# Performance work log

Measured on AMD Instinct MI355X. Metric: run time of the kernel, lower is better.

The kernel has to match this reference:

```python
import jax, jax.numpy as jnp
import numpy as np

DIM = 1024
NUM_HEADS = 16
HEAD_DIM = DIM // NUM_HEADS
SCALE = HEAD_DIM ** -0.5


def setup_inputs() -> dict:
    key = jax.random.key(0)
    k_x, k_qkv, k_pw, k_pb = jax.random.split(key, 4)
    B, L = 2, 2048
    x = jax.random.normal(k_x, (B, L, DIM), dtype=jnp.float32)
    # nn.Linear weights are [out, in]; stored the same way here.
    w_qkv = jax.random.normal(k_qkv, (3 * DIM, DIM), dtype=jnp.float32) * (DIM ** -0.5)
    w_proj = jax.random.normal(k_pw, (DIM, DIM), dtype=jnp.float32) * (DIM ** -0.5)
    b_proj = jax.random.normal(k_pb, (DIM,), dtype=jnp.float32) * 0.01
    return {"x": x, "w_qkv": w_qkv, "w_proj": w_proj, "b_proj": b_proj}


def reference(x, w_qkv, w_proj, b_proj):
    B, L, P = x.shape
    H, D = NUM_HEADS, HEAD_DIM
    # qkv projection (no bias): [B, L, 3*P]
    qkv = jnp.einsum('blp,op->blo', x, w_qkv)
    qkv = qkv.reshape(B, L, 3, H, D).transpose(2, 0, 3, 1, 4)  # [3, B, H, L, D]
    q, k, v = qkv[0], qkv[1], qkv[2]
    attn = jnp.einsum('bhld,bhmd->bhlm', q, k) * SCALE  # [B, H, L, L]
    attn = jax.nn.softmax(attn, axis=-1)
    out = jnp.einsum('bhlm,bhmd->bhld', attn, v)  # [B, H, L, D]
    out = out.transpose(0, 2, 1, 3).reshape(B, L, P)
    out = jnp.einsum('blp,op->blo', out, w_proj) + b_proj
    return out
```

## Files before the change

### kernel.cpp

```cpp
#include <hip/hip_runtime.h>
#include <hip/hip_bf16.h>
#include <stdint.h>
#include <stddef.h>

typedef short s16x8 __attribute__((ext_vector_type(8)));
typedef float f32x4  __attribute__((ext_vector_type(4)));
typedef float f32x16 __attribute__((ext_vector_type(16)));
typedef unsigned int u32x2 __attribute__((ext_vector_type(2)));

#define MFMA16(a, b, c) __builtin_amdgcn_mfma_f32_16x16x32_bf16((a), (b), (c), 0, 0, 0)
#define MFMA32(a, b, c) __builtin_amdgcn_mfma_f32_32x32x16_bf16((a), (b), (c), 0, 0, 0)
#define EXP2(x) __builtin_amdgcn_exp2f(x)
#define FMAX3(a, b, c) fmaxf(fmaxf((a), (b)), (c))

__device__ __forceinline__ unsigned short f2bf(float f) {
  union { float f; uint32_t u; } v; v.f = f;
  uint32_t u = v.u;
  return (unsigned short)((u + 0x7FFFu + ((u >> 16) & 1u)) >> 16);
}

__device__ __forceinline__ unsigned int pack_bf16x2(float a, float b) {
  __hip_bfloat162 h = __float22bfloat162_rn(make_float2(a, b));
  union { __hip_bfloat162 h; unsigned int u; } c; c.h = h;
  return c.u;
}

__device__ __forceinline__ void load_lds16(const void* gsrc, void* ldst) {
  void* gp = const_cast<void*>(gsrc);
  __builtin_amdgcn_global_load_lds(
      (__attribute__((address_space(1))) void*)gp,
      (__attribute__((address_space(3))) void*)ldst, 16, 0, 0);
}

#define B_    2
#define L_    2048
#define DIM_  1024
#define NH_   16
#define HD_   64
#define MTOT  (B_ * L_)
#define QSCALE_ 0.18033688011112042f

__global__ void cvt_all(const float* __restrict__ x, const float* __restrict__ wq,
                        const float* __restrict__ wp,
                        unsigned short* __restrict__ xb, unsigned short* __restrict__ wqb,
                        unsigned short* __restrict__ wpb) {
  const int X4 = 1048576, Q4 = 786432;
  int i = blockIdx.x * 256 + threadIdx.x;
  const float* in; unsigned short* out; int idx;
  if (i < X4)            { in = x;  out = xb;  idx = i; }
  else if (i < X4 + Q4)  { in = wq; out = wqb; idx = i - X4; }
  else                   { in = wp; out = wpb; idx = i - X4 - Q4; }
  float4 v = ((const float4*)in)[idx];
  uint2 r;
  r.x = pack_bf16x2(v.x, v.y);
  r.y = pack_bf16x2(v.z, v.w);
  ((uint2*)out)[idx] = r;
}

template <int EPI>
__global__ void __launch_bounds__(256)
gemm_bt(const unsigned short* __restrict__ A,
        const unsigned short* __restrict__ Bw,
        int M, int N, int K,
        unsigned short* __restrict__ Qb,
        unsigned short* __restrict__ Kb,
        unsigned short* __restrict__ Vt,
        float* __restrict__ Cout,
        const float* __restrict__ bias) {
  __shared__ __attribute__((aligned(16))) unsigned short Al[2][128 * 32];
  __shared__ __attribute__((aligned(16))) unsigned short Bl[2][128 * 32];
  const int tid  = threadIdx.x;
  const int lane = tid & 63, wv = tid >> 6;
  const int g = lane >> 4, lr = lane & 15;
  const int wr = wv >> 1, wc = wv & 1;
  const int m0 = blockIdx.x * 128, n0 = blockIdx.y * 128;

  f32x4 acc[4][4];
  const f32x4 zero = {0.f, 0.f, 0.f, 0.f};
#pragma unroll
  for (int i = 0; i < 4; i++)
#pragma unroll
    for (int j = 0; j < 4; j++) acc[i][j] = zero;

#define STAGE_G(buf, k0)                                                              \
  {                                                                                   \
    _Pragma("unroll")                                                                 \
    for (int pass = 0; pass < 2; ++pass) {                                            \
      int c   = pass * 256 + wv * 64 + lane;                                          \
      int row = c >> 2, kc = c & 3;                                                   \
      int ks  = (kc ^ ((row ^ (row >> 2)) & 3)) * 8;                                  \
      load_lds16(A  + (size_t)(m0 + row) * K + (k0) + ks, (char*)&Al[buf][0] + c * 16); \
      load_lds16(Bw + (size_t)(n0 + row) * K + (k0) + ks, (char*)&Bl[buf][0] + c * 16); \
    }                                                                                 \
  }

  STAGE_G(0, 0);
  __syncthreads();
  const int NTk = K >> 5;
  for (int t = 0; t < NTk; ++t) {
    const int cur = t & 1;
    if (t + 1 < NTk) STAGE_G(cur ^ 1, (t + 1) * 32);

    s16x8 af[4], bf[4];
#pragma unroll
    for (int mi = 0; mi < 4; mi++) {
      int row = wr * 64 + mi * 16 + lr;
      int ch  = g ^ ((row ^ (row >> 2)) & 3);
      af[mi]  = *(const s16x8*)((const char*)&Al[cur][0] + row * 64 + ch * 16);
    }
#pragma unroll
    for (int ni = 0; ni < 4; ni++) {
      int row = wc * 64 + ni * 16 + lr;
      int ch  = g ^ ((row ^ (row >> 2)) & 3);
      bf[ni]  = *(const s16x8*)((const char*)&Bl[cur][0] + row * 64 + ch * 16);
    }
#pragma unroll
    for (int mi = 0; mi < 4; mi++)
#pragma unroll
      for (int ni = 0; ni < 4; ni++)
        acc[mi][ni] = MFMA16(af[mi], bf[ni], acc[mi][ni]);
    __syncthreads();
  }
#undef STAGE_G

  if (EPI == 0) {
#pragma unroll
    for (int mi = 0; mi < 4; mi++)
#pragma unroll
      for (int ni = 0; ni < 4; ni++) {
        int ncol = n0 + wc * 64 + ni * 16 + lr;
        int s = ncol >> 10;
        int h = (ncol >> 6) & 15;
        int d = ncol & 63;
#pragma unroll
        for (int j = 0; j < 4; j++) {
          int m = m0 + wr * 64 + mi * 16 + g * 4 + j;
          int b = m >> 11, l = m & 2047;
          size_t bh = (size_t)(b * NH_ + h);
          if (s == 0)      Qb[(bh * L_ + l) * HD_ + d] = f2bf(acc[mi][ni][j] * QSCALE_);
          else if (s == 1) Kb[(bh * L_ + l) * HD_ + d] = f2bf(acc[mi][ni][j]);
          else             Vt[(bh * HD_ + d) * L_ + l] = f2bf(acc[mi][ni][j]);
        }
      }
  } else {
#pragma unroll
    for (int mi = 0; mi < 4; mi++)
#pragma unroll
      for (int ni = 0; ni < 4; ni++) {
        int ncol = n0 + wc * 64 + ni * 16 + lr;
        float bv = bias[ncol];
#pragma unroll
        for (int j = 0; j < 4; j++) {
          int m = m0 + wr * 64 + mi * 16 + g * 4 + j;
          Cout[(size_t)m * N + ncol] = acc[mi][ni][j] + bv;
        }
      }
  }
}

__global__ void __launch_bounds__(256)
attn_fwd(const unsigned short* __restrict__ Qb,
         const unsigned short* __restrict__ Kb,
         const unsigned short* __restrict__ Vt,
         unsigned short* __restrict__ Ob) {
  __shared__ __attribute__((aligned(16))) unsigned short Kl[2][64 * 64];
  __shared__ __attribute__((aligned(16))) unsigned short Vl[2][64 * 64];

  const int tid  = threadIdx.x;
  const int lane = tid & 63, wv = tid >> 6;
  const int hi = lane >> 5, lq = lane & 31;
  const int qt = blockIdx.x, bh = blockIdx.y;

  const unsigned short* Qh = Qb + (size_t)bh * L_ * HD_;
  const unsigned short* Kh = Kb + (size_t)bh * L_ * HD_;
  const unsigned short* Vh = Vt + (size_t)bh * HD_ * L_;
  const int q0 = qt * 128 + wv * 32;

  s16x8 qf[4];
#pragma unroll
  for (int ks = 0; ks < 4; ++ks)
    qf[ks] = *(const s16x8*)(Qh + (size_t)(q0 + lq) * HD_ + ks * 16 + hi * 8);

  s16x8 onesf;
#pragma unroll
  for (int e = 0; e < 8; ++e) onesf[e] = (short)0x3F80;

  f32x16 o0, o1, o2;
#pragma unroll
  for (int r = 0; r < 16; ++r) { o0[r] = 0.f; o1[r] = 0.f; o2[r] = 0.f; }
  float rm = -1e30f;

#define STAGE(buf, kv0)                                                          \
  {                                                                              \
    _Pragma("unroll")                                                            \
    for (int it = 0; it < 2; ++it) {                                             \
      int c = it * 256 + wv * 64 + lane;                                         \
      int row = c >> 3, cc = c & 7;                                              \
      int cs = (cc ^ (row & 7)) * 8;                                             \
      load_lds16(Kh + (size_t)((kv0) + row) * HD_ + cs, (char*)&Kl[buf][0] + c * 16); \
      load_lds16(Vh + (size_t)row * L_ + (kv0) + cs,    (char*)&Vl[buf][0] + c * 16); \
    }                                                                            \
  }

  STAGE(0, 0);
  __syncthreads();

  const int NT = L_ / 64;
  for (int t = 0; t < NT; ++t) {
    const int cur = t & 1;
    if (t + 1 < NT) STAGE(cur ^ 1, (t + 1) * 64);

    const unsigned short* KL = &Kl[cur][0];
    const unsigned short* VL = &Vl[cur][0];

    f32x16 s0, s1;
#pragma unroll
    for (int r = 0; r < 16; ++r) { s0[r] = 0.f; s1[r] = 0.f; }
    __builtin_amdgcn_s_setprio(1);
#pragma unroll
    for (int ks = 0; ks < 4; ++ks) {
      int cc = ((ks << 1) | hi) ^ (lq & 7);
      s16x8 k0 = *(const s16x8*)((const char*)KL + lq * 128 + cc * 16);
      s0 = MFMA32(k0, qf[ks], s0);
      s16x8 k1 = *(const s16x8*)((const char*)KL + (32 + lq) * 128 + cc * 16);
      s1 = MFMA32(k1, qf[ks], s1);
    }
    __builtin_amdgcn_s_setprio(0);

    float t0, t1, t2, t3, t4, t5;
    {
      float m01 = FMAX3(fmaxf(s0[0], s1[0]), fmaxf(s0[1], s1[1]), fmaxf(s0[2], s1[2]));
      float m02 = FMAX3(fmaxf(s0[3], s1[3]), fmaxf(s0[4], s1[4]), fmaxf(s0[5], s1[5]));
      float m03 = FMAX3(fmaxf(s0[6], s1[6]), fmaxf(s0[7], s1[7]), fmaxf(s0[8], s1[8]));
      float m04 = FMAX3(fmaxf(s0[9], s1[9]), fmaxf(s0[10], s1[10]), fmaxf(s0[11], s1[11]));
      float m05 = FMAX3(fmaxf(s0[12], s1[12]), fmaxf(s0[13], s1[13]), fmaxf(s0[14], s1[14]));
      float m06 = fmaxf(s0[15], s1[15]);
      t0 = FMAX3(m01, m02, m03);
      t1 = FMAX3(m04, m05, m06);
    }
    float pmh = fmaxf(t0, t1);
    union { float f; unsigned u; } cu; cu.f = pmh;
    u32x2 sw = __builtin_amdgcn_permlane32_swap(cu.u, cu.u, false, false);
    union { unsigned u; float f; } ca, cb; ca.u = sw[0]; cb.u = sw[1];
    float pm = fmaxf(ca.f, cb.f);

    float mn = rm;
    if (!__all(pm <= rm + 8.0f)) {
      mn = fmaxf(rm, pm);
      float al = EXP2(rm - mn);
#pragma unroll
      for (int r = 0; r < 16; ++r) { o0[r] *= al; o1[r] *= al; }
      o2[0] *= al;
      rm = mn;
    }

#pragma unroll
    for (int r = 0; r < 16; ++r) { s0[r] = EXP2(s0[r] - mn); s1[r] = EXP2(s1[r] - mn); }

#pragma unroll
    for (int st = 0; st < 2; ++st) {
      unsigned int pd[8];
#pragma unroll
      for (int r2 = 0; r2 < 8; ++r2)
        pd[r2] = st ? pack_bf16x2(s1[2 * r2], s1[2 * r2 + 1])
                    : pack_bf16x2(s0[2 * r2], s0[2 * r2 + 1]);
      __builtin_amdgcn_s_setprio(1);
#pragma unroll
      for (int ksl = 0; ksl < 2; ++ksl) {
        u32x2 e0 = __builtin_amdgcn_permlane32_swap(pd[4 * ksl + 0], pd[4 * ksl + 2], false, false);
        u32x2 e1 = __builtin_amdgcn_permlane32_swap(pd[4 * ksl + 1], pd[4 * ksl + 3], false, false);
        union { unsigned int u[4]; s16x8 v; } pa;
        pa.u[0] = e0[0];
        pa.u[1] = e1[0];
        pa.u[2] = e0[1];
        pa.u[3] = e1[1];
#pragma unroll
        for (int dt = 0; dt < 2; ++dt) {
          int row = dt * 32 + lq;
          int cc = (4 * st + 2 * ksl + hi) ^ (row & 7);
          s16x8 vf = *(const s16x8*)((const char*)VL + row * 128 + cc * 16);
          if (dt == 0) o0 = MFMA32(vf, pa.v, o0);
          else         o1 = MFMA32(vf, pa.v, o1);
        }
        o2 = MFMA32(onesf, pa.v, o2);
      }
      __builtin_amdgcn_s_setprio(0);
    }

    __syncthreads();
  }
#undef STAGE

  const int b = bh >> 4, h = bh & 15;
  const int q = q0 + lq;
  const float inv = 1.0f / o2[0];
  size_t base = ((size_t)(b * L_ + q)) * DIM_ + h * HD_;
#pragma unroll
  for (int dt = 0; dt < 2; ++dt)
#pragma unroll
    for (int r2 = 0; r2 < 8; ++r2) {
      int d = dt * 32 + 8 * (r2 >> 1) + 4 * hi + 2 * (r2 & 1);
      float a = (dt ? o1[2 * r2] : o0[2 * r2]) * inv;
      float c = (dt ? o1[2 * r2 + 1] : o0[2 * r2 + 1]) * inv;
      unsigned int pv = pack_bf16x2(a, c);
      *(unsigned int*)((unsigned short*)Ob + base + d) = pv;
    }
}

extern "C" void kernel_launch(void* const* d_in, const int* in_sizes, int n_in,
                              void* d_out, int out_size, void* d_ws, size_t ws_size,
                              hipStream_t stream) {
  const float* x      = (const float*)d_in[0];
  const float* w_qkv  = (const float*)d_in[1];
  const float* w_proj = (const float*)d_in[2];
  const float* b_proj = (const float*)d_in[3];
  float* out = (float*)d_out;

  const size_t N_X    = (size_t)MTOT * DIM_;
  const size_t N_WQKV = (size_t)3 * DIM_ * DIM_;
  const size_t N_WPRJ = (size_t)DIM_ * DIM_;
  const size_t N_QKV  = (size_t)B_ * NH_ * L_ * HD_;

  unsigned short* xb     = (unsigned short*)d_ws;
  unsigned short* wqkvb  = xb + N_X;
  unsigned short* wprojb = wqkvb + N_WQKV;
  unsigned short* Qb     = wprojb + N_WPRJ;
  unsigned short* Kb     = Qb + N_QKV;
  unsigned short* Vt     = Kb + N_QKV;
  unsigned short* Obuf   = Vt + N_QKV;

  cvt_all<<<8192, 256, 0, stream>>>(x, w_qkv, w_proj, xb, wqkvb, wprojb);

  dim3 g1(MTOT / 128, (3 * DIM_) / 128);
  gemm_bt<0><<<g1, 256, 0, stream>>>(xb, wqkvb, MTOT, 3 * DIM_, DIM_,
                                     Qb, Kb, Vt, nullptr, nullptr);

  dim3 g2(L_ / 128, B_ * NH_);
  attn_fwd<<<g2, 256, 0, stream>>>(Qb, Kb, Vt, Obuf);

  dim3 g3(MTOT / 128, DIM_ / 128);
  gemm_bt<1><<<g3, 256, 0, stream>>>(Obuf, wprojb, MTOT, DIM_, DIM_,
                                     nullptr, nullptr, nullptr, out, b_proj);
}
```

Baseline: 136.4 us.

## Triple-buffer LDS staging with explicit vmcnt waits and one barrier per iteration

Both the GEMM and attention kernels move from double to triple-buffered LDS tiles. Loads are issued two tiles ahead, and each iteration waits only for the older tile with s_waitcnt vmcnt, using a single raw barrier instead of two __syncthreads. This aims to hide global-to-LDS latency better and halve the barrier count. The cost is 50% more LDS per block, which may reduce occupancy, and the vmcnt(4) counting depends on the exact number of loads per stage. The GEMM MFMA block also gets raised wave priority.

```diff
diff --git a/kernel.cpp b/kernel.cpp
--- a/kernel.cpp
+++ b/kernel.cpp
@@ -12,6 +12,14 @@
 #define MFMA32(a, b, c) __builtin_amdgcn_mfma_f32_32x32x16_bf16((a), (b), (c), 0, 0, 0)
 #define EXP2(x) __builtin_amdgcn_exp2f(x)
 #define FMAX3(a, b, c) fmaxf(fmaxf((a), (b)), (c))
+
+#define WAITCNT_VM(N) asm volatile("s_waitcnt vmcnt(" #N ")" ::: "memory")
+#define BARRIER_RAW()                                  \
+  do {                                                 \
+    asm volatile("" ::: "memory");                     \
+    __builtin_amdgcn_s_barrier();                      \
+    asm volatile("" ::: "memory");                     \
+  } while (0)
 
 __device__ __forceinline__ unsigned short f2bf(float f) {
   union { float f; uint32_t u; } v; v.f = f;
@@ -67,8 +75,8 @@
         unsigned short* __restrict__ Vt,
         float* __restrict__ Cout,
         const float* __restrict__ bias) {
-  __shared__ __attribute__((aligned(16))) unsigned short Al[2][128 * 32];
-  __shared__ __attribute__((aligned(16))) unsigned short Bl[2][128 * 32];
+  __shared__ __attribute__((aligned(16))) unsigned short Al[3][128 * 32];
+  __shared__ __attribute__((aligned(16))) unsigned short Bl[3][128 * 32];
   const int tid  = threadIdx.x;
   const int lane = tid & 63, wv = tid >> 6;
   const int g = lane >> 4, lr = lane & 15;
@@ -95,11 +103,14 @@
   }
 
   STAGE_G(0, 0);
-  __syncthreads();
+  STAGE_G(1, 32);
   const int NTk = K >> 5;
   for (int t = 0; t < NTk; ++t) {
-    const int cur = t & 1;
-    if (t + 1 < NTk) STAGE_G(cur ^ 1, (t + 1) * 32);
+    if (t + 1 < NTk) WAITCNT_VM(4);
+    else             WAITCNT_VM(0);
+    BARRIER_RAW();
+    if (t + 2 < NTk) STAGE_G((t + 2) % 3, (t + 2) * 32);
+    const int cur = t % 3;
 
     s16x8 af[4], bf[4];
 #pragma unroll
@@ -114,12 +125,13 @@
       int ch  = g ^ ((row ^ (row >> 2)) & 3);
       bf[ni]  = *(const s16x8*)((const char*)&Bl[cur][0] + row * 64 + ch * 16);
     }
+    __builtin_amdgcn_s_setprio(1);
 #pragma unroll
     for (int mi = 0; mi < 4; mi++)
 #pragma unroll
       for (int ni = 0; ni < 4; ni++)
         acc[mi][ni] = MFMA16(af[mi], bf[ni], acc[mi][ni]);
-    __syncthreads();
+    __builtin_amdgcn_s_setprio(0);
   }
 #undef STAGE_G
 
@@ -163,8 +175,8 @@
          const unsigned short* __restrict__ Kb,
          const unsigned short* __restrict__ Vt,
          unsigned short* __restrict__ Ob) {
-  __shared__ __attribute__((aligned(16))) unsigned short Kl[2][64 * 64];
-  __shared__ __attribute__((aligned(16))) unsigned short Vl[2][64 * 64];
+  __shared__ __attribute__((aligned(16))) unsigned short Kl[3][64 * 64];
+  __shared__ __attribute__((aligned(16))) unsigned short Vl[3][64 * 64];
 
   const int tid  = threadIdx.x;
   const int lane = tid & 63, wv = tid >> 6;
@@ -203,15 +215,17 @@
   }
 
   STAGE(0, 0);
-  __syncthreads();
+  STAGE(1, 64);
 
   const int NT = L_ / 64;
   for (int t = 0; t < NT; ++t) {
-    const int cur = t & 1;
-    if (t + 1 < NT) STAGE(cur ^ 1, (t + 1) * 64);
-
-    const unsigned short* KL = &Kl[cur][0];
-    const unsigned short* VL = &Vl[cur][0];
+    if (t + 1 < NT) WAITCNT_VM(4);
+    else            WAITCNT_VM(0);
+    BARRIER_RAW();
+    if (t + 2 < NT) STAGE((t + 2) % 3, (t + 2) * 64);
+
+    const unsigned short* KL = &Kl[t % 3][0];
+    const unsigned short* VL = &Vl[t % 3][0];
 
     f32x16 s0, s1;
 #pragma unroll
@@ -227,7 +241,7 @@
     }
     __builtin_amdgcn_s_setprio(0);
 
-    float t0, t1, t2, t3, t4, t5;
+    float t0, t1;
     {
       float m01 = FMAX3(fmaxf(s0[0], s1[0]), fmaxf(s0[1], s1[1]), fmaxf(s0[2], s1[2]));
       float m02 = FMAX3(fmaxf(s0[3], s1[3]), fmaxf(s0[4], s1[4]), fmaxf(s0[5], s1[5]));
@@ -286,8 +300,6 @@
       }
       __builtin_amdgcn_s_setprio(0);
     }
-
-    __syncthreads();
   }
 #undef STAGE
 
```

New measurement: 141.9 us. 4.0% more time.

## Split attention KV range in two and merge partial outputs in a separate kernel

Applied to the files above, without the earlier changes.

The attention kernel now splits the key/value sequence into two halves along a new grid dimension, doubling the block count from 512 to 1024 so more of the GPU's compute units are occupied. Each half writes unnormalised bf16 partial outputs plus its running max and row sum to workspace. A new merge kernel combines the two halves with log-sum-exp weights and writes the normalised result. This adds an extra launch, extra global traffic for the partials, and an extra bf16 rounding of the unnormalised partials.

```diff
diff --git a/kernel.cpp b/kernel.cpp
--- a/kernel.cpp
+++ b/kernel.cpp
@@ -17,6 +17,10 @@
   union { float f; uint32_t u; } v; v.f = f;
   uint32_t u = v.u;
   return (unsigned short)((u + 0x7FFFu + ((u >> 16) & 1u)) >> 16);
+}
+
+__device__ __forceinline__ float bf2f(unsigned short u) {
+  union { uint32_t u; float f; } v; v.u = ((uint32_t)u) << 16; return v.f;
 }
 
 __device__ __forceinline__ unsigned int pack_bf16x2(float a, float b) {
@@ -38,6 +42,7 @@
 #define NH_   16
 #define HD_   64
 #define MTOT  (B_ * L_)
+#define ROWS_ 65536
 #define QSCALE_ 0.18033688011112042f
 
 __global__ void cvt_all(const float* __restrict__ x, const float* __restrict__ wq,
@@ -162,19 +167,21 @@
 attn_fwd(const unsigned short* __restrict__ Qb,
          const unsigned short* __restrict__ Kb,
          const unsigned short* __restrict__ Vt,
-         unsigned short* __restrict__ Ob) {
+         unsigned short* __restrict__ Opart,
+         float* __restrict__ Ml) {
   __shared__ __attribute__((aligned(16))) unsigned short Kl[2][64 * 64];
   __shared__ __attribute__((aligned(16))) unsigned short Vl[2][64 * 64];
 
   const int tid  = threadIdx.x;
   const int lane = tid & 63, wv = tid >> 6;
   const int hi = lane >> 5, lq = lane & 31;
-  const int qt = blockIdx.x, bh = blockIdx.y;
+  const int qt = blockIdx.x, bh = blockIdx.y, sp = blockIdx.z;
 
   const unsigned short* Qh = Qb + (size_t)bh * L_ * HD_;
   const unsigned short* Kh = Kb + (size_t)bh * L_ * HD_;
   const unsigned short* Vh = Vt + (size_t)bh * HD_ * L_;
   const int q0 = qt * 128 + wv * 32;
+  const int kvbase = sp * (L_ / 2);
 
   s16x8 qf[4];
 #pragma unroll
@@ -202,13 +209,13 @@
     }                                                                            \
   }
 
-  STAGE(0, 0);
+  STAGE(0, kvbase);
   __syncthreads();
 
-  const int NT = L_ / 64;
+  const int NT = (L_ / 2) / 64;
   for (int t = 0; t < NT; ++t) {
     const int cur = t & 1;
-    if (t + 1 < NT) STAGE(cur ^ 1, (t + 1) * 64);
+    if (t + 1 < NT) STAGE(cur ^ 1, kvbase + (t + 1) * 64);
 
     const unsigned short* KL = &Kl[cur][0];
     const unsigned short* VL = &Vl[cur][0];
@@ -227,7 +234,7 @@
     }
     __builtin_amdgcn_s_setprio(0);
 
-    float t0, t1, t2, t3, t4, t5;
+    float t0, t1;
     {
       float m01 = FMAX3(fmaxf(s0[0], s1[0]), fmaxf(s0[1], s1[1]), fmaxf(s0[2], s1[2]));
       float m02 = FMAX3(fmaxf(s0[3], s1[3]), fmaxf(s0[4], s1[4]), fmaxf(s0[5], s1[5]));
@@ -291,20 +298,51 @@
   }
 #undef STAGE
 
+  const int q = q0 + lq;
+  const size_t row = (size_t)bh * L_ + q;
+  unsigned short* Oprow = Opart + ((size_t)sp * ROWS_ + row) * 64;
+#pragma unroll
+  for (int grp = 0; grp < 4; ++grp) {
+    uint2 w0, w1;
+    w0.x = pack_bf16x2(o0[grp * 4 + 0], o0[grp * 4 + 1]);
+    w0.y = pack_bf16x2(o0[grp * 4 + 2], o0[grp * 4 + 3]);
+    *(uint2*)(Oprow + grp * 8 + 4 * hi) = w0;
+    w1.x = pack_bf16x2(o1[grp * 4 + 0], o1[grp * 4 + 1]);
+    w1.y = pack_bf16x2(o1[grp * 4 + 2], o1[grp * 4 + 3]);
+    *(uint2*)(Oprow + 32 + grp * 8 + 4 * hi) = w1;
+  }
+  if (hi == 0)
+    *(float2*)(Ml + ((size_t)sp * ROWS_ + row) * 2) = make_float2(rm, o2[0]);
+}
+
+__global__ void __launch_bounds__(256)
+attn_merge(const unsigned short* __restrict__ Opart, const float* __restrict__ Ml,
+           unsigned short* __restrict__ Ob) {
+  const int tid = threadIdx.x;
+  const int row = blockIdx.x * 16 + (tid >> 4);
+  const int dp  = (tid & 15) * 4;
+  const int bh = row >> 11, q = row & 2047;
   const int b = bh >> 4, h = bh & 15;
-  const int q = q0 + lq;
-  const float inv = 1.0f / o2[0];
-  size_t base = ((size_t)(b * L_ + q)) * DIM_ + h * HD_;
-#pragma unroll
-  for (int dt = 0; dt < 2; ++dt)
-#pragma unroll
-    for (int r2 = 0; r2 < 8; ++r2) {
-      int d = dt * 32 + 8 * (r2 >> 1) + 4 * hi + 2 * (r2 & 1);
-      float a = (dt ? o1[2 * r2] : o0[2 * r2]) * inv;
-      float c = (dt ? o1[2 * r2 + 1] : o0[2 * r2 + 1]) * inv;
-      unsigned int pv = pack_bf16x2(a, c);
-      *(unsigned int*)((unsigned short*)Ob + base + d) = pv;
-    }
+
+  float2 ml1 = *(const float2*)(Ml + (size_t)row * 2);
+  float2 ml2 = *(const float2*)(Ml + (size_t)(ROWS_ + row) * 2);
+  float m  = fmaxf(ml1.x, ml2.x);
+  float w1 = EXP2(ml1.x - m), w2 = EXP2(ml2.x - m);
+  float inv = 1.0f / (ml1.y * w1 + ml2.y * w2);
+  w1 *= inv; w2 *= inv;
+
+  const unsigned short* p1 = Opart + (size_t)row * 64 + dp;
+  const unsigned short* p2 = Opart + (size_t)ROWS_ * 64 + (size_t)row * 64 + dp;
+  ushort4 a = *(const ushort4*)p1;
+  ushort4 c = *(const ushort4*)p2;
+  float v0 = bf2f(a.x) * w1 + bf2f(c.x) * w2;
+  float v1 = bf2f(a.y) * w1 + bf2f(c.y) * w2;
+  float v2 = bf2f(a.z) * w1 + bf2f(c.z) * w2;
+  float v3 = bf2f(a.w) * w1 + bf2f(c.w) * w2;
+  uint2 w;
+  w.x = pack_bf16x2(v0, v1);
+  w.y = pack_bf16x2(v2, v3);
+  *(uint2*)(Ob + ((size_t)(b * L_ + q)) * DIM_ + h * HD_ + dp) = w;
 }
 
 extern "C" void kernel_launch(void* const* d_in, const int* in_sizes, int n_in,
@@ -328,6 +366,8 @@
   unsigned short* Kb     = Qb + N_QKV;
   unsigned short* Vt     = Kb + N_QKV;
   unsigned short* Obuf   = Vt + N_QKV;
+  unsigned short* Opart  = Obuf + N_X;
+  float*          Ml     = (float*)(Opart + (size_t)2 * ROWS_ * 64);
 
   cvt_all<<<8192, 256, 0, stream>>>(x, w_qkv, w_proj, xb, wqkvb, wprojb);
 
@@ -335,8 +375,10 @@
   gemm_bt<0><<<g1, 256, 0, stream>>>(xb, wqkvb, MTOT, 3 * DIM_, DIM_,
                                      Qb, Kb, Vt, nullptr, nullptr);
 
-  dim3 g2(L_ / 128, B_ * NH_);
-  attn_fwd<<<g2, 256, 0, stream>>>(Qb, Kb, Vt, Obuf);
+  dim3 g2(L_ / 128, B_ * NH_, 2);
+  attn_fwd<<<g2, 256, 0, stream>>>(Qb, Kb, Vt, Opart, Ml);
+
+  attn_merge<<<ROWS_ / 16, 256, 0, stream>>>(Opart, Ml, Obuf);
 
   dim3 g3(MTOT / 128, DIM_ / 128);
   gemm_bt<1><<<g3, 256, 0, stream>>>(Obuf, wprojb, MTOT, DIM_, DIM_,
```

Result: slower. 143.6 us (+5.3%).
